# Optimization experiments

Hardware: AMD Instinct MI355X
Metric: run time of the kernel (lower is better)

The kernel has to match this reference:

```python
import jax, jax.numpy as jnp
import numpy as np

N_NODES = 50000
N_EDGES = 800000
D_FEAT = 64


def setup_inputs() -> dict:
    key = jax.random.key(0)
    k1, k2, k3, k4 = jax.random.split(key, 4)
    x = jax.random.normal(k1, (N_NODES, D_FEAT), dtype=jnp.float32)
    e = jax.random.uniform(k2, (N_EDGES, 1), dtype=jnp.float32)
    src = jax.random.randint(k3, (N_EDGES,), 0, N_NODES, dtype=jnp.int32)
    dst = jax.random.randint(k4, (N_EDGES,), 0, N_NODES, dtype=jnp.int32)
    return {"t": 0, "x": x, "e": e, "src": src, "dst": dst}


def reference(t, x, e, src, dst):
    # u_mul_e: gather source node features and scale by edge weight -> [E, D]
    m = x[src] * e
    # fn.sum('m','x'): scatter-sum messages to destination nodes -> [N, D]
    out = jax.ops.segment_sum(m, dst, num_segments=N_NODES)
    return out
```

## Files before the change

kernel.cpp:

```cpp
#include <hip/hip_runtime.h>

#define N_NODES 50000
#define N_EDGES 800000
#define D_FEAT  64
#define NPB     128
#define NBINS   391
#define BINCAP  3072
#define EPB_A   4096
#define BLK_A   1024
#define KPT     (EPB_A / BLK_A)
#define CAPL    64
#define GPAD    16

__device__ __forceinline__ float bf16_to_f(unsigned short h) {
    return __uint_as_float(((unsigned int)h) << 16);
}
__device__ __forceinline__ unsigned short f_to_bf16_rne(float f) {
    unsigned int u = __float_as_uint(f);
    u += 0x7fffu + ((u >> 16) & 1u);
    return (unsigned short)(u >> 16);
}

__global__ __launch_bounds__(1024) void binscatter_kernel(
    const float4* __restrict__ x4,
    const float*  __restrict__ e,
    const int*    __restrict__ src,
    const int*    __restrict__ dst,
    int*          __restrict__ gcount,
    unsigned int* __restrict__ stage,
    ushort4*      __restrict__ xb4)
{
    __shared__ int bin_cnt[NBINS];
    __shared__ int bin_gbase[NBINS];

    int t = threadIdx.x;
    int base = blockIdx.x * EPB_A;

    for (int i = t; i < NBINS; i += BLK_A) bin_cnt[i] = 0;

    for (int k = 0; k < KPT; ++k) {
        int idx = base + k * BLK_A + t;
        if (idx < N_NODES * (D_FEAT / 4)) {
            float4 v = x4[idx];
            ushort4 h;
            h.x = f_to_bf16_rne(v.x); h.y = f_to_bf16_rne(v.y);
            h.z = f_to_bf16_rne(v.z); h.w = f_to_bf16_rne(v.w);
            xb4[idx] = h;
        }
    }
    __syncthreads();

    int          pd[KPT];
    unsigned int pr[KPT];
    int          pp[KPT];
    for (int k = 0; k < KPT; ++k) {
        int idx = base + k * BLK_A + t;
        pd[k] = -1;
        if (idx < N_EDGES) {
            int s = src[idx];
            int d = dst[idx];
            int wq = __float2int_rn(e[idx] * 511.0f);
            wq = wq < 0 ? 0 : (wq > 511 ? 511 : wq);
            pd[k] = d;
            pr[k] = ((unsigned int)s << 16) | ((unsigned int)(d & 127) << 9)
                  | (unsigned int)wq;
            pp[k] = atomicAdd(&bin_cnt[d >> 7], 1);
        }
    }
    __syncthreads();

    for (int i = t; i < NBINS; i += BLK_A)
        bin_gbase[i] = bin_cnt[i] ? atomicAdd(&gcount[i * GPAD], bin_cnt[i]) : 0;
    __syncthreads();

    for (int k = 0; k < KPT; ++k) {
        if (pd[k] >= 0) {
            int b   = pd[k] >> 7;
            int pos = bin_gbase[b] + pp[k];
            if (pos < BINCAP)
                stage[(size_t)b * BINCAP + pos] = pr[k];
        }
    }
}

__global__ __launch_bounds__(1024) void bin_reduce_kernel(
    const ushort4*      __restrict__ xb4,
    const int*          __restrict__ gcount,
    const unsigned int* __restrict__ stage,
    float4*             __restrict__ out4)
{
    __shared__ int          cnt[NPB];
    __shared__ unsigned int rec[NPB][CAPL];

    int b = blockIdx.x;
    int t = threadIdx.x;

    int m = gcount[b * GPAD];
    if (m > BINCAP) m = BINCAP;

    unsigned int r0 = 0, r1 = 0, r2 = 0;
    const unsigned int* sb = stage + (size_t)b * BINCAP;
    if (t < m)        r0 = sb[t];
    if (t + 1024 < m) r1 = sb[t + 1024];
    if (t + 2048 < m) r2 = sb[t + 2048];

    {
        unsigned long long* p = (unsigned long long*)&rec[0][0];
        #pragma unroll
        for (int k = 0; k < 4; ++k) p[t + k * 1024] = 0ull;
        if (t < NPB) cnt[t] = 0;
    }
    __syncthreads();

    if (t < m)        { int dl = (r0 >> 9) & 127; int p0 = atomicAdd(&cnt[dl], 1); if (p0 < CAPL) rec[dl][p0] = r0; }
    if (t + 1024 < m) { int dl = (r1 >> 9) & 127; int p1 = atomicAdd(&cnt[dl], 1); if (p1 < CAPL) rec[dl][p1] = r1; }
    if (t + 2048 < m) { int dl = (r2 >> 9) & 127; int p2 = atomicAdd(&cnt[dl], 1); if (p2 < CAPL) rec[dl][p2] = r2; }
    __syncthreads();

    int lane = t & 63;
    int wv   = t >> 6;
    int q    = lane >> 4;
    int sub  = lane & 15;

#define CHUNK2(BASE)                                                          \
    {                                                                         \
        unsigned int a0 = rec[nlA][(BASE) + q];                               \
        unsigned int a1 = rec[nlA][(BASE) + 4 + q];                           \
        unsigned int a2 = rec[nlA][(BASE) + 8 + q];                           \
        unsigned int a3 = rec[nlA][(BASE) + 12 + q];                          \
        unsigned int b0 = rec[nlB][(BASE) + q];                               \
        unsigned int b1 = rec[nlB][(BASE) + 4 + q];                           \
        unsigned int b2 = rec[nlB][(BASE) + 8 + q];                           \
        unsigned int b3 = rec[nlB][(BASE) + 12 + q];                          \
        ushort4 hA0 = xb4[(size_t)(a0 >> 16) * 16 + sub];                     \
        ushort4 hA1 = xb4[(size_t)(a1 >> 16) * 16 + sub];                     \
        ushort4 hA2 = xb4[(size_t)(a2 >> 16) * 16 + sub];                     \
        ushort4 hA3 = xb4[(size_t)(a3 >> 16) * 16 + sub];                     \
        ushort4 hB0 = xb4[(size_t)(b0 >> 16) * 16 + sub];                     \
        ushort4 hB1 = xb4[(size_t)(b1 >> 16) * 16 + sub];                     \
        ushort4 hB2 = xb4[(size_t)(b2 >> 16) * 16 + sub];                     \
        ushort4 hB3 = xb4[(size_t)(b3 >> 16) * 16 + sub];                     \
        float wA0 = (float)(a0 & 511u) * (1.0f / 511.0f);                     \
        float wA1 = (float)(a1 & 511u) * (1.0f / 511.0f);                     \
        float wA2 = (float)(a2 & 511u) * (1.0f / 511.0f);                     \
        float wA3 = (float)(a3 & 511u) * (1.0f / 511.0f);                     \
        float wB0 = (float)(b0 & 511u) * (1.0f / 511.0f);                     \
        float wB1 = (float)(b1 & 511u) * (1.0f / 511.0f);                     \
        float wB2 = (float)(b2 & 511u) * (1.0f / 511.0f);                     \
        float wB3 = (float)(b3 & 511u) * (1.0f / 511.0f);                     \
        aA.x += wA0 * bf16_to_f(hA0.x) + wA1 * bf16_to_f(hA1.x)               \
              + wA2 * bf16_to_f(hA2.x) + wA3 * bf16_to_f(hA3.x);              \
        aA.y += wA0 * bf16_to_f(hA0.y) + wA1 * bf16_to_f(hA1.y)               \
              + wA2 * bf16_to_f(hA2.y) + wA3 * bf16_to_f(hA3.y);              \
        aA.z += wA0 * bf16_to_f(hA0.z) + wA1 * bf16_to_f(hA1.z)               \
              + wA2 * bf16_to_f(hA2.z) + wA3 * bf16_to_f(hA3.z);              \
        aA.w += wA0 * bf16_to_f(hA0.w) + wA1 * bf16_to_f(hA1.w)               \
              + wA2 * bf16_to_f(hA2.w) + wA3 * bf16_to_f(hA3.w);              \
        aB.x += wB0 * bf16_to_f(hB0.x) + wB1 * bf16_to_f(hB1.x)               \
              + wB2 * bf16_to_f(hB2.x) + wB3 * bf16_to_f(hB3.x);              \
        aB.y += wB0 * bf16_to_f(hB0.y) + wB1 * bf16_to_f(hB1.y)               \
              + wB2 * bf16_to_f(hB2.y) + wB3 * bf16_to_f(hB3.y);              \
        aB.z += wB0 * bf16_to_f(hB0.z) + wB1 * bf16_to_f(hB1.z)               \
              + wB2 * bf16_to_f(hB2.z) + wB3 * bf16_to_f(hB3.z);              \
        aB.w += wB0 * bf16_to_f(hB0.w) + wB1 * bf16_to_f(hB1.w)               \
              + wB2 * bf16_to_f(hB2.w) + wB3 * bf16_to_f(hB3.w);              \
    }

    for (int k = 0; k < 8; k += 2) {
        int nlA = wv * 8 + k;
        int nlB = nlA + 1;
        int nA  = b * NPB + nlA;
        int nB  = nA + 1;
        if (nA >= N_NODES) break;
        bool validB = (nB < N_NODES);

        int cA = cnt[nlA]; if (cA > CAPL) cA = CAPL;
        int cB = validB ? cnt[nlB] : 0; if (cB > CAPL) cB = CAPL;
        int cmax = cA > cB ? cA : cB;

        float4 aA = make_float4(0.f, 0.f, 0.f, 0.f);
        float4 aB = make_float4(0.f, 0.f, 0.f, 0.f);

        CHUNK2(0);
        if (cmax > 16) CHUNK2(16);
        if (cmax > 32) CHUNK2(32);
        if (cmax > 48) CHUNK2(48);

        aA.x += __shfl_xor(aA.x, 16); aA.y += __shfl_xor(aA.y, 16);
        aA.z += __shfl_xor(aA.z, 16); aA.w += __shfl_xor(aA.w, 16);
        aA.x += __shfl_xor(aA.x, 32); aA.y += __shfl_xor(aA.y, 32);
        aA.z += __shfl_xor(aA.z, 32); aA.w += __shfl_xor(aA.w, 32);
        aB.x += __shfl_xor(aB.x, 16); aB.y += __shfl_xor(aB.y, 16);
        aB.z += __shfl_xor(aB.z, 16); aB.w += __shfl_xor(aB.w, 16);
        aB.x += __shfl_xor(aB.x, 32); aB.y += __shfl_xor(aB.y, 32);
        aB.z += __shfl_xor(aB.z, 32); aB.w += __shfl_xor(aB.w, 32);

        if (q == 0) {
            out4[(size_t)nA * 16 + sub] = aA;
            if (validB) out4[(size_t)nB * 16 + sub] = aB;
        }
    }
#undef CHUNK2
}

__global__ __launch_bounds__(256) void scatter_add_kernel(
    const float* __restrict__ x,
    const float* __restrict__ e,
    const int*   __restrict__ src,
    const int*   __restrict__ dst,
    float*       __restrict__ out)
{
    long long idx = (long long)blockIdx.x * blockDim.x + threadIdx.x;
    if (idx >= (long long)N_EDGES * (D_FEAT / 4)) return;
    int edge = (int)(idx >> 4);
    int c    = (int)(idx & 15);
    int   s = src[edge];
    int   d = dst[edge];
    float w = e[edge];
    const float4* x4 = (const float4*)x;
    float4 v = x4[(long long)s * (D_FEAT / 4) + c];
    float* o = out + (long long)d * D_FEAT + c * 4;
    atomicAdd(o + 0, v.x * w);
    atomicAdd(o + 1, v.y * w);
    atomicAdd(o + 2, v.z * w);
    atomicAdd(o + 3, v.w * w);
}

extern "C" void kernel_launch(void* const* d_in, const int* in_sizes, int n_in,
                              void* d_out, int out_size, void* d_ws, size_t ws_size,
                              hipStream_t stream)
{
    const float* x   = (const float*)d_in[1];
    const float* e   = (const float*)d_in[2];
    const int*   src = (const int*)d_in[3];
    const int*   dst = (const int*)d_in[4];
    float*       out = (float*)d_out;

    size_t off_gcount = 0;
    size_t off_stage  = off_gcount + (size_t)NBINS * GPAD * sizeof(int);
    size_t off_xb     = off_stage + (size_t)NBINS * BINCAP * sizeof(unsigned int);
    size_t need       = off_xb + (size_t)N_NODES * D_FEAT * sizeof(unsigned short);

    if (ws_size >= need) {
        int*          gcount = (int*)((char*)d_ws + off_gcount);
        unsigned int* stage  = (unsigned int*)((char*)d_ws + off_stage);
        ushort4*      xb4    = (ushort4*)((char*)d_ws + off_xb);

        hipMemsetAsync(gcount, 0, (size_t)NBINS * GPAD * sizeof(int), stream);

        int gridA = (N_EDGES + EPB_A - 1) / EPB_A;
        binscatter_kernel<<<gridA, BLK_A, 0, stream>>>(
            (const float4*)x, e, src, dst, gcount, stage, xb4);

        int gridB = NBINS;
        bin_reduce_kernel<<<gridB, 1024, 0, stream>>>(
            xb4, gcount, stage, (float4*)out);
    } else {
        hipMemsetAsync(out, 0, (size_t)out_size * sizeof(float), stream);
        long long total = (long long)N_EDGES * (D_FEAT / 4);
        int block = 256;
        int grid  = (int)((total + block - 1) / block);
        scatter_add_kernel<<<grid, block, 0, stream>>>(x, e, src, dst, out);
    }
}
```

Baseline: 110.0 us.

## Fuse bin scatter and bin reduce into one cooperative persistent kernel

Replaces the memset plus two-kernel pipeline with a single cooperative kernel of 256 blocks that zeroes the bin counters, converts x to bf16, bins edges, and reduces bins, separated by grid-wide syncs. Each block now handles 3125 edges and 3125 float4 chunks of x, and the reduce phase loops over bins with stride GRID. The aim is to remove the launch and memset overhead and the gaps between kernels. In exchange it adds two grid.sync barriers, reuses shared memory through a union, and leaves 135 blocks reducing a second bin, so the reduce phase has a tail.

```diff
diff --git a/kernel.cpp b/kernel.cpp
--- a/kernel.cpp
+++ b/kernel.cpp
@@ -1,4 +1,7 @@
 #include <hip/hip_runtime.h>
+#include <hip/hip_cooperative_groups.h>
+
+namespace cg = cooperative_groups;
 
 #define N_NODES 50000
 #define N_EDGES 800000
@@ -6,9 +9,10 @@
 #define NPB     128
 #define NBINS   391
 #define BINCAP  3072
-#define EPB_A   4096
-#define BLK_A   1024
-#define KPT     (EPB_A / BLK_A)
+#define GRID    256
+#define BLK     1024
+#define EPB     3125
+#define KPT     4
 #define CAPL    64
 #define GPAD    16
 
@@ -21,26 +25,36 @@
     return (unsigned short)(u >> 16);
 }
 
-__global__ __launch_bounds__(1024) void binscatter_kernel(
+__global__ __launch_bounds__(BLK) void fused_kernel(
     const float4* __restrict__ x4,
     const float*  __restrict__ e,
     const int*    __restrict__ src,
     const int*    __restrict__ dst,
     int*          __restrict__ gcount,
     unsigned int* __restrict__ stage,
-    ushort4*      __restrict__ xb4)
+    ushort4*      __restrict__ xb4,
+    float4*       __restrict__ out4)
 {
-    __shared__ int bin_cnt[NBINS];
-    __shared__ int bin_gbase[NBINS];
-
-    int t = threadIdx.x;
-    int base = blockIdx.x * EPB_A;
-
-    for (int i = t; i < NBINS; i += BLK_A) bin_cnt[i] = 0;
-
-    for (int k = 0; k < KPT; ++k) {
-        int idx = base + k * BLK_A + t;
-        if (idx < N_NODES * (D_FEAT / 4)) {
+    __shared__ union {
+        struct { int bin_cnt[NBINS]; int bin_gbase[NBINS]; } a;
+        struct { int cnt[NPB]; unsigned int rec[NPB][CAPL]; } r;
+    } sh;
+
+    cg::grid_group grid = cg::this_grid();
+    int t    = threadIdx.x;
+    int b    = blockIdx.x;
+    int base = b * EPB;
+    int lim  = base + EPB;
+
+    if (t < 2) {
+        int i = b + t * GRID;
+        if (i < NBINS) gcount[i * GPAD] = 0;
+    }
+    for (int i = t; i < NBINS; i += BLK) sh.a.bin_cnt[i] = 0;
+
+    for (int k = 0; k < KPT; ++k) {
+        int idx = base + k * BLK + t;
+        if (idx < lim) {
             float4 v = x4[idx];
             ushort4 h;
             h.x = f_to_bf16_rne(v.x); h.y = f_to_bf16_rne(v.y);
@@ -54,9 +68,9 @@
     unsigned int pr[KPT];
     int          pp[KPT];
     for (int k = 0; k < KPT; ++k) {
-        int idx = base + k * BLK_A + t;
+        int idx = base + k * BLK + t;
         pd[k] = -1;
-        if (idx < N_EDGES) {
+        if (idx < lim) {
             int s = src[idx];
             int d = dst[idx];
             int wq = __float2int_rn(e[idx] * 511.0f);
@@ -64,46 +78,205 @@
             pd[k] = d;
             pr[k] = ((unsigned int)s << 16) | ((unsigned int)(d & 127) << 9)
                   | (unsigned int)wq;
+            pp[k] = atomicAdd(&sh.a.bin_cnt[d >> 7], 1);
+        }
+    }
+    __syncthreads();
+    __threadfence();
+    grid.sync();
+
+    for (int i = t; i < NBINS; i += BLK)
+        sh.a.bin_gbase[i] = sh.a.bin_cnt[i]
+                          ? atomicAdd(&gcount[i * GPAD], sh.a.bin_cnt[i]) : 0;
+    __syncthreads();
+
+    for (int k = 0; k < KPT; ++k) {
+        if (pd[k] >= 0) {
+            int bb  = pd[k] >> 7;
+            int pos = sh.a.bin_gbase[bb] + pp[k];
+            if (pos < BINCAP)
+                stage[(size_t)bb * BINCAP + pos] = pr[k];
+        }
+    }
+    __threadfence();
+    grid.sync();
+
+    int lane = t & 63;
+    int wv   = t >> 6;
+    int q    = lane >> 4;
+    int sub  = lane & 15;
+
+    for (int bb = b; bb < NBINS; bb += GRID) {
+        int m = gcount[bb * GPAD];
+        if (m > BINCAP) m = BINCAP;
+
+        unsigned int r0 = 0, r1 = 0, r2 = 0;
+        const unsigned int* sb = stage + (size_t)bb * BINCAP;
+        if (t < m)        r0 = sb[t];
+        if (t + 1024 < m) r1 = sb[t + 1024];
+        if (t + 2048 < m) r2 = sb[t + 2048];
+        __syncthreads();
+
+        {
+            unsigned long long* p = (unsigned long long*)&sh.r.rec[0][0];
+            #pragma unroll
+            for (int k = 0; k < 4; ++k) p[t + k * 1024] = 0ull;
+            if (t < NPB) sh.r.cnt[t] = 0;
+        }
+        __syncthreads();
+
+        if (t < m)        { int dl = (r0 >> 9) & 127; int p0 = atomicAdd(&sh.r.cnt[dl], 1); if (p0 < CAPL) sh.r.rec[dl][p0] = r0; }
+        if (t + 1024 < m) { int dl = (r1 >> 9) & 127; int p1 = atomicAdd(&sh.r.cnt[dl], 1); if (p1 < CAPL) sh.r.rec[dl][p1] = r1; }
+        if (t + 2048 < m) { int dl = (r2 >> 9) & 127; int p2 = atomicAdd(&sh.r.cnt[dl], 1); if (p2 < CAPL) sh.r.rec[dl][p2] = r2; }
+        __syncthreads();
+
+#define CHUNK2(BASE)                                                          \
+        {                                                                     \
+            unsigned int a0 = sh.r.rec[nlA][(BASE) + q];                      \
+            unsigned int a1 = sh.r.rec[nlA][(BASE) + 4 + q];                  \
+            unsigned int a2 = sh.r.rec[nlA][(BASE) + 8 + q];                  \
+            unsigned int a3 = sh.r.rec[nlA][(BASE) + 12 + q];                 \
+            unsigned int b0 = sh.r.rec[nlB][(BASE) + q];                      \
+            unsigned int b1 = sh.r.rec[nlB][(BASE) + 4 + q];                  \
+            unsigned int b2 = sh.r.rec[nlB][(BASE) + 8 + q];                  \
+            unsigned int b3 = sh.r.rec[nlB][(BASE) + 12 + q];                 \
+            ushort4 hA0 = xb4[(size_t)(a0 >> 16) * 16 + sub];                 \
+            ushort4 hA1 = xb4[(size_t)(a1 >> 16) * 16 + sub];                 \
+            ushort4 hA2 = xb4[(size_t)(a2 >> 16) * 16 + sub];                 \
+            ushort4 hA3 = xb4[(size_t)(a3 >> 16) * 16 + sub];                 \
+            ushort4 hB0 = xb4[(size_t)(b0 >> 16) * 16 + sub];                 \
+            ushort4 hB1 = xb4[(size_t)(b1 >> 16) * 16 + sub];                 \
+            ushort4 hB2 = xb4[(size_t)(b2 >> 16) * 16 + sub];                 \
+            ushort4 hB3 = xb4[(size_t)(b3 >> 16) * 16 + sub];                 \
+            float wA0 = (float)(a0 & 511u) * (1.0f / 511.0f);                 \
+            float wA1 = (float)(a1 & 511u) * (1.0f / 511.0f);                 \
+            float wA2 = (float)(a2 & 511u) * (1.0f / 511.0f);                 \
+            float wA3 = (float)(a3 & 511u) * (1.0f / 511.0f);                 \
+            float wB0 = (float)(b0 & 511u) * (1.0f / 511.0f);                 \
+            float wB1 = (float)(b1 & 511u) * (1.0f / 511.0f);                 \
+            float wB2 = (float)(b2 & 511u) * (1.0f / 511.0f);                 \
+            float wB3 = (float)(b3 & 511u) * (1.0f / 511.0f);                 \
+            aA.x += wA0 * bf16_to_f(hA0.x) + wA1 * bf16_to_f(hA1.x)           \
+                  + wA2 * bf16_to_f(hA2.x) + wA3 * bf16_to_f(hA3.x);          \
+            aA.y += wA0 * bf16_to_f(hA0.y) + wA1 * bf16_to_f(hA1.y)           \
+                  + wA2 * bf16_to_f(hA2.y) + wA3 * bf16_to_f(hA3.y);          \
+            aA.z += wA0 * bf16_to_f(hA0.z) + wA1 * bf16_to_f(hA1.z)           \
+                  + wA2 * bf16_to_f(hA2.z) + wA3 * bf16_to_f(hA3.z);          \
+            aA.w += wA0 * bf16_to_f(hA0.w) + wA1 * bf16_to_f(hA1.w)           \
+                  + wA2 * bf16_to_f(hA2.w) + wA3 * bf16_to_f(hA3.w);          \
+            aB.x += wB0 * bf16_to_f(hB0.x) + wB1 * bf16_to_f(hB1.x)           \
+                  + wB2 * bf16_to_f(hB2.x) + wB3 * bf16_to_f(hB3.x);          \
+            aB.y += wB0 * bf16_to_f(hB0.y) + wB1 * bf16_to_f(hB1.y)           \
+                  + wB2 * bf16_to_f(hB2.y) + wB3 * bf16_to_f(hB3.y);          \
+            aB.z += wB0 * bf16_to_f(hB0.z) + wB1 * bf16_to_f(hB1.z)           \
+                  + wB2 * bf16_to_f(hB2.z) + wB3 * bf16_to_f(hB3.z);          \
+            aB.w += wB0 * bf16_to_f(hB0.w) + wB1 * bf16_to_f(hB1.w)           \
+                  + wB2 * bf16_to_f(hB2.w) + wB3 * bf16_to_f(hB3.w);          \
+        }
+
+        for (int k = 0; k < 8; k += 2) {
+            int nlA = wv * 8 + k;
+            int nlB = nlA + 1;
+            int nA  = bb * NPB + nlA;
+            int nB  = nA + 1;
+            if (nA < N_NODES) {
+                bool validB = (nB < N_NODES);
+
+                int cA = sh.r.cnt[nlA]; if (cA > CAPL) cA = CAPL;
+                int cB = validB ? sh.r.cnt[nlB] : 0; if (cB > CAPL) cB = CAPL;
+                int cmax = cA > cB ? cA : cB;
+
+                float4 aA = make_float4(0.f, 0.f, 0.f, 0.f);
+                float4 aB = make_float4(0.f, 0.f, 0.f, 0.f);
+
+                CHUNK2(0);
+                if (cmax > 16) CHUNK2(16);
+                if (cmax > 32) CHUNK2(32);
+                if (cmax > 48) CHUNK2(48);
+
+                aA.x += __shfl_xor(aA.x, 16); aA.y += __shfl_xor(aA.y, 16);
+                aA.z += __shfl_xor(aA.z, 16); aA.w += __shfl_xor(aA.w, 16);
+                aA.x += __shfl_xor(aA.x, 32); aA.y += __shfl_xor(aA.y, 32);
+                aA.z += __shfl_xor(aA.z, 32); aA.w += __shfl_xor(aA.w, 32);
+                aB.x += __shfl_xor(aB.x, 16); aB.y += __shfl_xor(aB.y, 16);
+                aB.z += __shfl_xor(aB.z, 16); aB.w += __shfl_xor(aB.w, 16);
+                aB.x += __shfl_xor(aB.x, 32); aB.y += __shfl_xor(aB.y, 32);
+                aB.z += __shfl_xor(aB.z, 32); aB.w += __shfl_xor(aB.w, 32);
+
+                if (q == 0) {
+                    out4[(size_t)nA * 16 + sub] = aA;
+                    if (validB) out4[(size_t)nB * 16 + sub] = aB;
+                }
+            }
+        }
+#undef CHUNK2
+    }
+}
+
+__global__ __launch_bounds__(1024) void binscatter_kernel(
+    const float4* __restrict__ x4, const float* __restrict__ e,
+    const int* __restrict__ src, const int* __restrict__ dst,
+    int* __restrict__ gcount, unsigned int* __restrict__ stage,
+    ushort4* __restrict__ xb4)
+{
+    __shared__ int bin_cnt[NBINS];
+    __shared__ int bin_gbase[NBINS];
+    int t = threadIdx.x;
+    int base = blockIdx.x * EPB;
+    int lim  = base + EPB;
+    for (int i = t; i < NBINS; i += BLK) bin_cnt[i] = 0;
+    for (int k = 0; k < KPT; ++k) {
+        int idx = base + k * BLK + t;
+        if (idx < lim) {
+            float4 v = x4[idx];
+            ushort4 h;
+            h.x = f_to_bf16_rne(v.x); h.y = f_to_bf16_rne(v.y);
+            h.z = f_to_bf16_rne(v.z); h.w = f_to_bf16_rne(v.w);
+            xb4[idx] = h;
+        }
+    }
+    __syncthreads();
+    int pd[KPT]; unsigned int pr[KPT]; int pp[KPT];
+    for (int k = 0; k < KPT; ++k) {
+        int idx = base + k * BLK + t;
+        pd[k] = -1;
+        if (idx < lim) {
+            int s = src[idx]; int d = dst[idx];
+            int wq = __float2int_rn(e[idx] * 511.0f);
+            wq = wq < 0 ? 0 : (wq > 511 ? 511 : wq);
+            pd[k] = d;
+            pr[k] = ((unsigned int)s << 16) | ((unsigned int)(d & 127) << 9) | (unsigned int)wq;
             pp[k] = atomicAdd(&bin_cnt[d >> 7], 1);
         }
     }
     __syncthreads();
-
-    for (int i = t; i < NBINS; i += BLK_A)
+    for (int i = t; i < NBINS; i += BLK)
         bin_gbase[i] = bin_cnt[i] ? atomicAdd(&gcount[i * GPAD], bin_cnt[i]) : 0;
     __syncthreads();
-
     for (int k = 0; k < KPT; ++k) {
         if (pd[k] >= 0) {
-            int b   = pd[k] >> 7;
-            int pos = bin_gbase[b] + pp[k];
-            if (pos < BINCAP)
-                stage[(size_t)b * BINCAP + pos] = pr[k];
+            int bb = pd[k] >> 7;
+            int pos = bin_gbase[bb] + pp[k];
+            if (pos < BINCAP) stage[(size_t)bb * BINCAP + pos] = pr[k];
         }
     }
 }
 
 __global__ __launch_bounds__(1024) void bin_reduce_kernel(
-    const ushort4*      __restrict__ xb4,
-    const int*          __restrict__ gcount,
-    const unsigned int* __restrict__ stage,
-    float4*             __restrict__ out4)
+    const ushort4* __restrict__ xb4, const int* __restrict__ gcount,
+    const unsigned int* __restrict__ stage, float4* __restrict__ out4)
 {
     __shared__ int          cnt[NPB];
     __shared__ unsigned int rec[NPB][CAPL];
-
     int b = blockIdx.x;
     int t = threadIdx.x;
-
     int m = gcount[b * GPAD];
     if (m > BINCAP) m = BINCAP;
-
     unsigned int r0 = 0, r1 = 0, r2 = 0;
     const unsigned int* sb = stage + (size_t)b * BINCAP;
     if (t < m)        r0 = sb[t];
     if (t + 1024 < m) r1 = sb[t + 1024];
     if (t + 2048 < m) r2 = sb[t + 2048];
-
     {
         unsigned long long* p = (unsigned long long*)&rec[0][0];
         #pragma unroll
@@ -111,81 +284,69 @@
         if (t < NPB) cnt[t] = 0;
     }
     __syncthreads();
-
     if (t < m)        { int dl = (r0 >> 9) & 127; int p0 = atomicAdd(&cnt[dl], 1); if (p0 < CAPL) rec[dl][p0] = r0; }
     if (t + 1024 < m) { int dl = (r1 >> 9) & 127; int p1 = atomicAdd(&cnt[dl], 1); if (p1 < CAPL) rec[dl][p1] = r1; }
     if (t + 2048 < m) { int dl = (r2 >> 9) & 127; int p2 = atomicAdd(&cnt[dl], 1); if (p2 < CAPL) rec[dl][p2] = r2; }
     __syncthreads();
-
-    int lane = t & 63;
-    int wv   = t >> 6;
-    int q    = lane >> 4;
-    int sub  = lane & 15;
-
-#define CHUNK2(BASE)                                                          \
-    {                                                                         \
-        unsigned int a0 = rec[nlA][(BASE) + q];                               \
-        unsigned int a1 = rec[nlA][(BASE) + 4 + q];                           \
-        unsigned int a2 = rec[nlA][(BASE) + 8 + q];                           \
-        unsigned int a3 = rec[nlA][(BASE) + 12 + q];                          \
-        unsigned int b0 = rec[nlB][(BASE) + q];                               \
-        unsigned int b1 = rec[nlB][(BASE) + 4 + q];                           \
-        unsigned int b2 = rec[nlB][(BASE) + 8 + q];                           \
-        unsigned int b3 = rec[nlB][(BASE) + 12 + q];                          \
-        ushort4 hA0 = xb4[(size_t)(a0 >> 16) * 16 + sub];                     \
-        ushort4 hA1 = xb4[(size_t)(a1 >> 16) * 16 + sub];                     \
-        ushort4 hA2 = xb4[(size_t)(a2 >> 16) * 16 + sub];                     \
-        ushort4 hA3 = xb4[(size_t)(a3 >> 16) * 16 + sub];                     \
-        ushort4 hB0 = xb4[(size_t)(b0 >> 16) * 16 + sub];                     \
-        ushort4 hB1 = xb4[(size_t)(b1 >> 16) * 16 + sub];                     \
-        ushort4 hB2 = xb4[(size_t)(b2 >> 16) * 16 + sub];                     \
-        ushort4 hB3 = xb4[(size_t)(b3 >> 16) * 16 + sub];                     \
-        float wA0 = (float)(a0 & 511u) * (1.0f / 511.0f);                     \
-        float wA1 = (float)(a1 & 511u) * (1.0f / 511.0f);                     \
-        float wA2 = (float)(a2 & 511u) * (1.0f / 511.0f);                     \
-        float wA3 = (float)(a3 & 511u) * (1.0f / 511.0f);                     \
-        float wB0 = (float)(b0 & 511u) * (1.0f / 511.0f);                     \
-        float wB1 = (float)(b1 & 511u) * (1.0f / 511.0f);                     \
-        float wB2 = (float)(b2 & 511u) * (1.0f / 511.0f);                     \
-        float wB3 = (float)(b3 & 511u) * (1.0f / 511.0f);                     \
-        aA.x += wA0 * bf16_to_f(hA0.x) + wA1 * bf16_to_f(hA1.x)               \
-              + wA2 * bf16_to_f(hA2.x) + wA3 * bf16_to_f(hA3.x);              \
-        aA.y += wA0 * bf16_to_f(hA0.y) + wA1 * bf16_to_f(hA1.y)               \
-              + wA2 * bf16_to_f(hA2.y) + wA3 * bf16_to_f(hA3.y);              \
-        aA.z += wA0 * bf16_to_f(hA0.z) + wA1 * bf16_to_f(hA1.z)               \
-              + wA2 * bf16_to_f(hA2.z) + wA3 * bf16_to_f(hA3.z);              \
-        aA.w += wA0 * bf16_to_f(hA0.w) + wA1 * bf16_to_f(hA1.w)               \
-              + wA2 * bf16_to_f(hA2.w) + wA3 * bf16_to_f(hA3.w);              \
-        aB.x += wB0 * bf16_to_f(hB0.x) + wB1 * bf16_to_f(hB1.x)               \
-              + wB2 * bf16_to_f(hB2.x) + wB3 * bf16_to_f(hB3.x);              \
-        aB.y += wB0 * bf16_to_f(hB0.y) + wB1 * bf16_to_f(hB1.y)               \
-              + wB2 * bf16_to_f(hB2.y) + wB3 * bf16_to_f(hB3.y);              \
-        aB.z += wB0 * bf16_to_f(hB0.z) + wB1 * bf16_to_f(hB1.z)               \
-              + wB2 * bf16_to_f(hB2.z) + wB3 * bf16_to_f(hB3.z);              \
-        aB.w += wB0 * bf16_to_f(hB0.w) + wB1 * bf16_to_f(hB1.w)               \
-              + wB2 * bf16_to_f(hB2.w) + wB3 * bf16_to_f(hB3.w);              \
-    }
-
+    int lane = t & 63, wv = t >> 6, q = lane >> 4, sub = lane & 15;
     for (int k = 0; k < 8; k += 2) {
-        int nlA = wv * 8 + k;
-        int nlB = nlA + 1;
-        int nA  = b * NPB + nlA;
-        int nB  = nA + 1;
+        int nlA = wv * 8 + k, nlB = nlA + 1;
+        int nA = b * NPB + nlA, nB = nA + 1;
         if (nA >= N_NODES) break;
         bool validB = (nB < N_NODES);
-
         int cA = cnt[nlA]; if (cA > CAPL) cA = CAPL;
         int cB = validB ? cnt[nlB] : 0; if (cB > CAPL) cB = CAPL;
         int cmax = cA > cB ? cA : cB;
-
         float4 aA = make_float4(0.f, 0.f, 0.f, 0.f);
         float4 aB = make_float4(0.f, 0.f, 0.f, 0.f);
-
-        CHUNK2(0);
-        if (cmax > 16) CHUNK2(16);
-        if (cmax > 32) CHUNK2(32);
-        if (cmax > 48) CHUNK2(48);
-
+#define CHUNK2F(BASE)                                                         \
+        {                                                                     \
+            unsigned int a0 = rec[nlA][(BASE) + q];                           \
+            unsigned int a1 = rec[nlA][(BASE) + 4 + q];                       \
+            unsigned int a2 = rec[nlA][(BASE) + 8 + q];                       \
+            unsigned int a3 = rec[nlA][(BASE) + 12 + q];                      \
+            unsigned int b0 = rec[nlB][(BASE) + q];                           \
+            unsigned int b1 = rec[nlB][(BASE) + 4 + q];                       \
+            unsigned int b2 = rec[nlB][(BASE) + 8 + q];                       \
+            unsigned int b3 = rec[nlB][(BASE) + 12 + q];                      \
+            ushort4 hA0 = xb4[(size_t)(a0 >> 16) * 16 + sub];                 \
+            ushort4 hA1 = xb4[(size_t)(a1 >> 16) * 16 + sub];                 \
+            ushort4 hA2 = xb4[(size_t)(a2 >> 16) * 16 + sub];                 \
+            ushort4 hA3 = xb4[(size_t)(a3 >> 16) * 16 + sub];                 \
+            ushort4 hB0 = xb4[(size_t)(b0 >> 16) * 16 + sub];                 \
+            ushort4 hB1 = xb4[(size_t)(b1 >> 16) * 16 + sub];                 \
+            ushort4 hB2 = xb4[(size_t)(b2 >> 16) * 16 + sub];                 \
+            ushort4 hB3 = xb4[(size_t)(b3 >> 16) * 16 + sub];                 \
+            float wA0 = (float)(a0 & 511u) * (1.0f / 511.0f);                 \
+            float wA1 = (float)(a1 & 511u) * (1.0f / 511.0f);                 \
+            float wA2 = (float)(a2 & 511u) * (1.0f / 511.0f);                 \
+            float wA3 = (float)(a3 & 511u) * (1.0f / 511.0f);                 \
+            float wB0 = (float)(b0 & 511u) * (1.0f / 511.0f);                 \
+            float wB1 = (float)(b1 & 511u) * (1.0f / 511.0f);                 \
+            float wB2 = (float)(b2 & 511u) * (1.0f / 511.0f);                 \
+            float wB3 = (float)(b3 & 511u) * (1.0f / 511.0f);                 \
+            aA.x += wA0 * bf16_to_f(hA0.x) + wA1 * bf16_to_f(hA1.x)           \
+                  + wA2 * bf16_to_f(hA2.x) + wA3 * bf16_to_f(hA3.x);          \
+            aA.y += wA0 * bf16_to_f(hA0.y) + wA1 * bf16_to_f(hA1.y)           \
+                  + wA2 * bf16_to_f(hA2.y) + wA3 * bf16_to_f(hA3.y);          \
+            aA.z += wA0 * bf16_to_f(hA0.z) + wA1 * bf16_to_f(hA1.z)           \
+                  + wA2 * bf16_to_f(hA2.z) + wA3 * bf16_to_f(hA3.z);          \
+            aA.w += wA0 * bf16_to_f(hA0.w) + wA1 * bf16_to_f(hA1.w)           \
+                  + wA2 * bf16_to_f(hA2.w) + wA3 * bf16_to_f(hA3.w);          \
+            aB.x += wB0 * bf16_to_f(hB0.x) + wB1 * bf16_to_f(hB1.x)           \
+                  + wB2 * bf16_to_f(hB2.x) + wB3 * bf16_to_f(hB3.x);          \
+            aB.y += wB0 * bf16_to_f(hB0.y) + wB1 * bf16_to_f(hB1.y)           \
+                  + wB2 * bf16_to_f(hB2.y) + wB3 * bf16_to_f(hB3.y);          \
+            aB.z += wB0 * bf16_to_f(hB0.z) + wB1 * bf16_to_f(hB1.z)           \
+                  + wB2 * bf16_to_f(hB2.z) + wB3 * bf16_to_f(hB3.z);          \
+            aB.w += wB0 * bf16_to_f(hB0.w) + wB1 * bf16_to_f(hB1.w)           \
+                  + wB2 * bf16_to_f(hB2.w) + wB3 * bf16_to_f(hB3.w);          \
+        }
+        CHUNK2F(0);
+        if (cmax > 16) CHUNK2F(16);
+        if (cmax > 32) CHUNK2F(32);
+        if (cmax > 48) CHUNK2F(48);
+#undef CHUNK2F
         aA.x += __shfl_xor(aA.x, 16); aA.y += __shfl_xor(aA.y, 16);
         aA.z += __shfl_xor(aA.z, 16); aA.w += __shfl_xor(aA.w, 16);
         aA.x += __shfl_xor(aA.x, 32); aA.y += __shfl_xor(aA.y, 32);
@@ -194,21 +355,17 @@
         aB.z += __shfl_xor(aB.z, 16); aB.w += __shfl_xor(aB.w, 16);
         aB.x += __shfl_xor(aB.x, 32); aB.y += __shfl_xor(aB.y, 32);
         aB.z += __shfl_xor(aB.z, 32); aB.w += __shfl_xor(aB.w, 32);
-
         if (q == 0) {
             out4[(size_t)nA * 16 + sub] = aA;
             if (validB) out4[(size_t)nB * 16 + sub] = aB;
         }
     }
-#undef CHUNK2
 }
 
 __global__ __launch_bounds__(256) void scatter_add_kernel(
-    const float* __restrict__ x,
-    const float* __restrict__ e,
-    const int*   __restrict__ src,
-    const int*   __restrict__ dst,
-    float*       __restrict__ out)
+    const float* __restrict__ x, const float* __restrict__ e,
+    const int* __restrict__ src, const int* __restrict__ dst,
+    float* __restrict__ out)
 {
     long long idx = (long long)blockIdx.x * blockDim.x + threadIdx.x;
     if (idx >= (long long)N_EDGES * (D_FEAT / 4)) return;
@@ -246,15 +403,21 @@
         unsigned int* stage  = (unsigned int*)((char*)d_ws + off_stage);
         ushort4*      xb4    = (ushort4*)((char*)d_ws + off_xb);
 
-        hipMemsetAsync(gcount, 0, (size_t)NBINS * GPAD * sizeof(int), stream);
-
-        int gridA = (N_EDGES + EPB_A - 1) / EPB_A;
-        binscatter_kernel<<<gridA, BLK_A, 0, stream>>>(
-            (const float4*)x, e, src, dst, gcount, stage, xb4);
-
-        int gridB = NBINS;
-        bin_reduce_kernel<<<gridB, 1024, 0, stream>>>(
-            xb4, gcount, stage, (float4*)out);
+        const float4* x4p  = (const float4*)x;
+        float4*       out4 = (float4*)out;
+        void* args[] = { (void*)&x4p, (void*)&e, (void*)&src, (void*)&dst,
+                         (void*)&gcount, (void*)&stage, (void*)&xb4, (void*)&out4 };
+
+        hipError_t err = hipLaunchCooperativeKernel(
+            (void*)fused_kernel, dim3(GRID), dim3(BLK), args, 0, stream);
+
+        if (err != hipSuccess) {
+            hipMemsetAsync(gcount, 0, (size_t)NBINS * GPAD * sizeof(int), stream);
+            binscatter_kernel<<<GRID, BLK, 0, stream>>>(
+                x4p, e, src, dst, gcount, stage, xb4);
+            bin_reduce_kernel<<<NBINS, BLK, 0, stream>>>(
+                xb4, gcount, stage, out4);
+        }
     } else {
         hipMemsetAsync(out, 0, (size_t)out_size * sizeof(float), stream);
         long long total = (long long)N_EDGES * (D_FEAT / 4);
```

Measured after the change: 375.2 us. +241.1%, slower.
